# Kernel optimization log

Measured on AMD Instinct MI355X. Metric: run time of the kernel, lower is better.

## Reference

```python
import jax, jax.numpy as jnp
import numpy as np
import math

V, B, C, H, W, D, G, N = 4, 2, 32, 128, 128, 32, 8, 4
ATTN_TEMP = 2.0


def _bilinear_sample(img, gx, gy):
    """img: (C,Hs,Ws); gx,gy: (P,) normalized coords in [-1,1].
    PyTorch grid_sample(mode=bilinear, padding=zeros, align_corners=True)."""
    Cc, Hs, Ws = img.shape
    x = (gx + 1.0) * 0.5 * (Ws - 1)
    y = (gy + 1.0) * 0.5 * (Hs - 1)
    x0 = jnp.floor(x)
    y0 = jnp.floor(y)
    wx = x - x0
    wy = y - y0
    x0i = x0.astype(jnp.int32)
    y0i = y0.astype(jnp.int32)

    def gather(xi, yi):
        valid = ((xi >= 0) & (xi < Ws) & (yi >= 0) & (yi < Hs)).astype(img.dtype)
        v = img[:, jnp.clip(yi, 0, Hs - 1), jnp.clip(xi, 0, Ws - 1)]
        return v * valid

    v00 = gather(x0i, y0i)
    v01 = gather(x0i + 1, y0i)
    v10 = gather(x0i, y0i + 1)
    v11 = gather(x0i + 1, y0i + 1)
    return (v00 * (1 - wx) + v01 * wx) * (1 - wy) + (v10 * (1 - wx) + v11 * wx) * wy


_bilinear_batched = jax.vmap(_bilinear_sample)  # over batch


def _homo_warp(src_fea, src_proj, ref_proj, depth):
    """src_fea (B,C,Hs,Ws), projs (B,4,4), depth (B,D,H,W) -> (B,C,D,H,W)."""
    Bb, Cc, Hs, Ws = src_fea.shape
    Dd, Hr, Wr = depth.shape[1], depth.shape[2], depth.shape[3]
    proj = src_proj @ jnp.linalg.inv(ref_proj)
    rot = proj[:, :3, :3]
    trans = proj[:, :3, 3]  # (B,3)
    yy, xx = jnp.meshgrid(jnp.arange(Hr, dtype=jnp.float32),
                          jnp.arange(Wr, dtype=jnp.float32), indexing='ij')
    xyz = jnp.stack([xx.ravel(), yy.ravel(), jnp.ones(Hr * Wr, jnp.float32)], 0)  # (3,P)
    rot_xyz = jnp.einsum('bij,jp->bip', rot, xyz)  # (B,3,P)
    pts = rot_xyz[:, :, None, :] * depth.reshape(Bb, 1, Dd, Hr * Wr) \
          + trans[:, :, None, None]  # (B,3,D,P)
    z = pts[:, 2]
    z = jnp.where(z == 0.0, 1e-9, z)
    gx = pts[:, 0] / z / ((Ws - 1) / 2.0) - 1.0  # (B,D,P)
    gy = pts[:, 1] / z / ((Hs - 1) / 2.0) - 1.0
    # grid built under torch.no_grad in the original
    gx = jax.lax.stop_gradient(gx).reshape(Bb, Dd * Hr * Wr)
    gy = jax.lax.stop_gradient(gy).reshape(Bb, Dd * Hr * Wr)
    warped = _bilinear_batched(src_fea, gx, gy)  # (B,C,D*P)
    return warped.reshape(Bb, Cc, Dd, Hr, Wr)


def setup_inputs() -> dict:
    key = jax.random.key(0)
    ks = jax.random.split(key, 6)
    ref_features = jax.random.normal(ks[0], (V, B, C, H, W), jnp.float32)
    src_features = jax.random.normal(ks[1], (V, B, C, H, W), jnp.float32)
    # structured camera matrices: [.,.,0]=extrinsic, [.,.,1]=intrinsic
    f = 100.0
    K = np.eye(4, dtype=np.float32)
    K[0, 0] = f; K[1, 1] = f; K[0, 2] = W / 2.0; K[1, 2] = H / 2.0
    projs = np.zeros((B, V + 1, 2, 4, 4), np.float32)
    for v in range(V + 1):
        ang = 0.0 if v == 0 else 0.02 * v
        ca, sa = math.cos(ang), math.sin(ang)
        E = np.eye(4, dtype=np.float32)
        E[:3, :3] = np.array([[ca, 0, sa], [0, 1, 0], [-sa, 0, ca]], np.float32)
        E[0, 3] = 0.0 if v == 0 else 5.0 * v
        projs[:, v, 0] = E
        projs[:, v, 1] = K
    proj_matrices = jnp.asarray(projs)
    dvals = jnp.linspace(425.0, 935.0, D, dtype=jnp.float32)
    depth_hypo = dvals[None, :, None, None] * jnp.ones((B, D, H, W), jnp.float32)
    sample_grids = 2.0 * jax.random.uniform(ks[2], (V, B, N, H, W, 2), jnp.float32) - 1.0
    w_reg = jax.random.normal(ks[3], (G,), jnp.float32) * 0.1
    w_enh = jax.random.normal(ks[4], (G, G * N), jnp.float32) * 0.05
    return {
        'ref_features': ref_features,
        'src_features': src_features,
        'proj_matrices': proj_matrices,
        'depth_hypo': depth_hypo,
        'sample_grids': sample_grids,
        'w_reg': w_reg,
        'w_enh': w_enh,
        'group_cor_dim': G,
        'stage_idx': 3,
    }


def reference(ref_features, src_features, proj_matrices, depth_hypo,
              sample_grids, w_reg, w_enh, group_cor_dim, stage_idx):
    Bb, Dd, Hh, Ww = depth_hypo.shape
    Cc = ref_features.shape[2]
    Gg = group_cor_dim
    ref_proj = proj_matrices[:, 0]
    ref_proj_new = ref_proj[:, 0].at[:, :3, :4].set(
        jnp.einsum('bij,bjk->bik', ref_proj[:, 1, :3, :3], ref_proj[:, 0, :3, :4]))
    cor_weight_sum = 1e-8
    cor_feats = 0.0
    cor_weights = []
    for src_idx in range(V):
        src_proj = proj_matrices[:, src_idx + 1]
        src_proj_new = src_proj[:, 0].at[:, :3, :4].set(
            jnp.einsum('bij,bjk->bik', src_proj[:, 1, :3, :3], src_proj[:, 0, :3, :4]))
        warped_src = _homo_warp(src_features[src_idx], src_proj_new, ref_proj_new,
                                depth_hypo)  # (B,C,D,H,W)
        ref_vol = ref_features[src_idx][:, :, None].reshape(Bb, Gg, Cc // Gg, 1, Hh, Ww)
        wsrc = warped_src.reshape(Bb, Gg, Cc // Gg, Dd, Hh, Ww)
        cor_feat = (wsrc * ref_vol).mean(2)  # (B,G,D,H,W) group correlation
        # --- regcorr: second grid_sample along epipolar-line samples ---
        cf = cor_feat.reshape(Bb, Gg * Dd, Hh, Ww)
        grids = sample_grids[src_idx].reshape(Bb, N * Hh * Ww, 2)
        cf_s = _bilinear_batched(cf, grids[..., 0], grids[..., 1])  # (B,G*D,N*H*W)
        cf_s = cf_s.reshape(Bb, Gg, Dd, N, Hh, Ww)
        cf_s = jnp.transpose(cf_s, (0, 1, 3, 2, 4, 5)).reshape(Bb, Gg * N, Dd, Hh, Ww)
        # line_cross_enhanced_net stand-in: learned mix of line samples, residual add
        cor_feat = cor_feat + jnp.einsum('gk,bkdhw->bgdhw', w_enh, cf_s)
        # --- attn_fuse_d softmax fusion across depth ---
        cor_weight = jax.nn.softmax(cor_feat.sum(1) / ATTN_TEMP, axis=1) / math.sqrt(Cc)
        cor_weight_sum = cor_weight_sum + cor_weight
        cor_weights.append(cor_weight.max(1))
        cor_feats = cor_feats + cor_weight[:, None] * cor_feat
    cor_feats = cor_feats / cor_weight_sum[:, None]
    # regnet stand-in: linear reduction over group dim
    attn_logits = jnp.einsum('g,bgdhw->bdhw', w_reg, cor_feats)
    attn_weight = jax.nn.softmax(attn_logits, axis=1)
    idx = jnp.argmax(attn_weight, axis=1)  # (B,H,W)
    depth = jnp.take_along_axis(depth_hypo, idx[:, None], axis=1)[:, 0]
    # stage_idx=3 -> interpolate scale_factor=1 (identity)
    photometric_confidence = attn_weight.max(1)
    return depth, photometric_confidence, attn_weight, jnp.stack(cor_weights)
```

## Files before the change

kernel.cpp:

```cpp
#include <hip/hip_runtime.h>

#define Vv 4
#define Bn 2
#define Cn 32
#define Hn 128
#define Wn 128
#define Dn 32
#define Gn 8
#define Nn 4
#define HW (Hn*Wn)
#define BHW (Bn*Hn*Wn)
#define DHW (Dn*Hn*Wn)
#define BDHW (Bn*Dn*Hn*Wn)
#define NBLK (DHW/256)
#define WBLK (DHW/512)
#define RBLK (Gn*HW/256)
#define NST  (Vv*Bn)

__global__ void setup_proj(const float* __restrict__ pm,
                           const float* __restrict__ wenh,
                           const float* __restrict__ wreg,
                           double* __restrict__ projws,
                           double* __restrict__ wtab) {
    int t = threadIdx.x;
    if (t < Gn) wtab[t] = (double)wreg[t];
    if (t < Gn * Nn) {
        double a = 0.0, c = 0.0;
        for (int g = 0; g < Gn; g++) {
            double wv = (double)wenh[g * (Gn * Nn) + t];
            a += wv;
            c += (double)wreg[g] * wv;
        }
        wtab[8 + t] = a; wtab[40 + t] = c;
    }
    if (t >= Vv * Bn) return;
    int v = t / Bn, b = t % Bn;
    const float* Eref = pm + (((size_t)b * (Vv + 1) + 0) * 2 + 0) * 16;
    const float* Kref = pm + (((size_t)b * (Vv + 1) + 0) * 2 + 1) * 16;
    const float* Esrc = pm + (((size_t)b * (Vv + 1) + (v + 1)) * 2 + 0) * 16;
    const float* Ksrc = pm + (((size_t)b * (Vv + 1) + (v + 1)) * 2 + 1) * 16;
    double R[16], S[16];
    for (int r = 0; r < 3; r++)
        for (int c = 0; c < 4; c++) {
            R[r*4+c] = (double)Kref[r*4+0]*Eref[0*4+c] + (double)Kref[r*4+1]*Eref[1*4+c] + (double)Kref[r*4+2]*Eref[2*4+c];
            S[r*4+c] = (double)Ksrc[r*4+0]*Esrc[0*4+c] + (double)Ksrc[r*4+1]*Esrc[1*4+c] + (double)Ksrc[r*4+2]*Esrc[2*4+c];
        }
    for (int c = 0; c < 4; c++) { R[12+c] = Eref[12+c]; S[12+c] = Esrc[12+c]; }
    double M[4][8];
    for (int r = 0; r < 4; r++)
        for (int c = 0; c < 4; c++) { M[r][c] = R[r*4+c]; M[r][4+c] = (r == c) ? 1.0 : 0.0; }
    for (int col = 0; col < 4; col++) {
        int piv = col; double best = fabs(M[col][col]);
        for (int r = col+1; r < 4; r++) { double a = fabs(M[r][col]); if (a > best) { best = a; piv = r; } }
        if (piv != col)
            for (int c = 0; c < 8; c++) { double tmp = M[col][c]; M[col][c] = M[piv][c]; M[piv][c] = tmp; }
        double inv = 1.0 / M[col][col];
        for (int c = 0; c < 8; c++) M[col][c] *= inv;
        for (int r = 0; r < 4; r++) if (r != col) {
            double f = M[r][col];
            for (int c = 0; c < 8; c++) M[r][c] -= f * M[col][c];
        }
    }
    double P[16];
    for (int r = 0; r < 4; r++)
        for (int c = 0; c < 4; c++) {
            double acc = 0.0;
            for (int k = 0; k < 4; k++) acc += S[r*4+k] * M[k][4+c];
            P[r*4+c] = acc;
        }
    double* o = projws + t * 12;
    o[0]=P[0];  o[1]=P[1];  o[2]=P[2];
    o[3]=P[4];  o[4]=P[5];  o[5]=P[6];
    o[6]=P[8];  o[7]=P[9];  o[8]=P[10];
    o[9]=P[3];  o[10]=P[7]; o[11]=P[11];
}

__device__ __forceinline__ void repack_body(
    int tid, const float* __restrict__ srcf, const float* __restrict__ reff,
    float4* __restrict__ qsrc, float4* __restrict__ qref, int v, int b)
{
    int p = tid & (HW - 1);
    int g = tid >> 14;
    const float* sb = srcf + ((size_t)(v*Bn + b)) * Cn * HW + (size_t)(g*4) * HW + p;
    const float* rb = reff + ((size_t)(v*Bn + b)) * Cn * HW + (size_t)(g*4) * HW + p;
    float4 s4; s4.x = sb[0]; s4.y = sb[HW]; s4.z = sb[2*HW]; s4.w = sb[3*HW];
    float4 r4; r4.x = rb[0]; r4.y = rb[HW]; r4.z = rb[2*HW]; r4.w = rb[3*HW];
    qsrc[(size_t)g * HW + p] = s4;
    qref[(size_t)g * HW + p] = r4;
}

__device__ __forceinline__ void warp_bin_q(
    int d, int p, double bx, double by, double bz,
    const float4* __restrict__ qsrc, const float4* __restrict__ qref,
    const float* __restrict__ dh, const double* __restrict__ pr,
    const float* sU1, const float* sU2, const float* sR,
    float2* __restrict__ ownbuf, float2* __restrict__ tapbuf, int b)
{
    double depth = (double)dh[(size_t)(b * Dn + d) * HW + p];
    double px = bx * depth + pr[9];
    double py = by * depth + pr[10];
    double pz = bz * depth + pr[11];
    if (pz == 0.0) pz = 1e-9;
    double invz = 1.0 / pz;
    double xs = px * invz;
    double ys = py * invz;
    double x0f = floor(xs), y0f = floor(ys);
    double wx = xs - x0f, wy = ys - y0f;
    int ix = (int)x0f, iy = (int)y0f;
    bool vx0 = (ix >= 0) && (ix < Wn), vx1 = (ix + 1 >= 0) && (ix + 1 < Wn);
    bool vy0 = (iy >= 0) && (iy < Hn), vy1 = (iy + 1 >= 0) && (iy + 1 < Hn);
    int cx0 = min(max(ix, 0), Wn-1), cx1 = min(max(ix+1, 0), Wn-1);
    int cy0 = min(max(iy, 0), Hn-1), cy1 = min(max(iy+1, 0), Hn-1);
    float a00 = (vx0 && vy0) ? (float)((1.0-wx)*(1.0-wy)) : 0.f;
    float a01 = (vx1 && vy0) ? (float)(wx*(1.0-wy))       : 0.f;
    float a10 = (vx0 && vy1) ? (float)((1.0-wx)*wy)       : 0.f;
    float a11 = (vx1 && vy1) ? (float)(wx*wy)             : 0.f;
    int o00 = cy0*Wn + cx0, o01 = cy0*Wn + cx1, o10 = cy1*Wn + cx0, o11 = cy1*Wn + cx1;
    float cor[Gn];
    #pragma unroll
    for (int half = 0; half < 2; half++) {
        float4 T00[4], T01[4], T10[4], T11[4];
        #pragma unroll
        for (int j2 = 0; j2 < 4; j2++) {
            const float4* qs = qsrc + (size_t)(half*4 + j2) * HW;
            T00[j2] = qs[o00]; T01[j2] = qs[o01];
            T10[j2] = qs[o10]; T11[j2] = qs[o11];
        }
        #pragma unroll
        for (int j2 = 0; j2 < 4; j2++) {
            int j = half*4 + j2;
            float4 rr = qref[(size_t)j * HW + p];
            float vx = a00*T00[j2].x + a01*T01[j2].x + a10*T10[j2].x + a11*T11[j2].x;
            float vy = a00*T00[j2].y + a01*T01[j2].y + a10*T10[j2].y + a11*T11[j2].y;
            float vz = a00*T00[j2].z + a01*T01[j2].z + a10*T10[j2].z + a11*T11[j2].z;
            float vw = a00*T00[j2].w + a01*T01[j2].w + a10*T10[j2].w + a11*T11[j2].w;
            cor[j] = ((vx*rr.x + vy*rr.y) + vz*rr.z) + vw*rr.w;
        }
    }
    float s_own = 0.f, r_own = 0.f;
    #pragma unroll
    for (int g = 0; g < Gn; g++) { s_own += cor[g]; r_own += sR[g] * cor[g]; }
    float2 o2; o2.x = 0.25f * s_own; o2.y = 0.25f * r_own;
    ownbuf[(size_t)p * Dn + d] = o2;
    #pragma unroll
    for (int n = 0; n < Nn; n++) {
        float t1 = 0.f, t2 = 0.f;
        #pragma unroll
        for (int g = 0; g < Gn; g++) {
            t1 += sU1[g*Nn + n] * cor[g];
            t2 += sU2[g*Nn + n] * cor[g];
        }
        float2 t; t.x = 0.25f * t1; t.y = 0.25f * t2;
        tapbuf[((size_t)p * Nn + n) * Dn + d] = t;
    }
}

__device__ __forceinline__ void warp_body_q2(
    int tid, const float4* __restrict__ qsrc, const float4* __restrict__ qref,
    const float* __restrict__ dh, const double* __restrict__ projws,
    const float* sU1, const float* sU2, const float* sR,
    float2* __restrict__ ownbuf, float2* __restrict__ tapbuf, int v, int b)
{
    int dlo = tid & 15, p = tid >> 4;
    int w = p & 127, h = p >> 7;
    const double* pr = projws + (v * Bn + b) * 12;
    double xf = (double)w, yf = (double)h;
    double bx = pr[0]*xf + pr[1]*yf + pr[2];
    double by = pr[3]*xf + pr[4]*yf + pr[5];
    double bz = pr[6]*xf + pr[7]*yf + pr[8];
    #pragma unroll
    for (int e = 0; e < 2; e++)
        warp_bin_q(dlo + 16*e, p, bx, by, bz, qsrc, qref, dh, pr,
                   sU1, sU2, sR, ownbuf, tapbuf, b);
}

__device__ __forceinline__ void warp_body(
    int tid, const float* __restrict__ srcf, const float* __restrict__ reff,
    const float* __restrict__ dh, const double* __restrict__ projws,
    const float* sU1, const float* sU2, const float* sR,
    float2* __restrict__ ownbuf, float2* __restrict__ tapbuf, int v, int b)
{
    int d = tid & 31, p = tid >> 5;
    int w = p & 127, h = p >> 7;
    const double* pr = projws + (v * Bn + b) * 12;
    double depth = (double)dh[(size_t)(b * Dn + d) * HW + p];
    double xf = (double)w, yf = (double)h;
    double px = (pr[0]*xf + pr[1]*yf + pr[2]) * depth + pr[9];
    double py = (pr[3]*xf + pr[4]*yf + pr[5]) * depth + pr[10];
    double pz = (pr[6]*xf + pr[7]*yf + pr[8]) * depth + pr[11];
    if (pz == 0.0) pz = 1e-9;
    double invz = 1.0 / pz;
    double xs = px * invz;
    double ys = py * invz;
    double x0f = floor(xs), y0f = floor(ys);
    double wx = xs - x0f, wy = ys - y0f;
    int ix = (int)x0f, iy = (int)y0f;
    bool vx0 = (ix >= 0) && (ix < Wn), vx1 = (ix + 1 >= 0) && (ix + 1 < Wn);
    bool vy0 = (iy >= 0) && (iy < Hn), vy1 = (iy + 1 >= 0) && (iy + 1 < Hn);
    int cx0 = min(max(ix, 0), Wn-1), cx1 = min(max(ix+1, 0), Wn-1);
    int cy0 = min(max(iy, 0), Hn-1), cy1 = min(max(iy+1, 0), Hn-1);
    float a00 = (vx0 && vy0) ? (float)((1.0-wx)*(1.0-wy)) : 0.f;
    float a01 = (vx1 && vy0) ? (float)(wx*(1.0-wy))       : 0.f;
    float a10 = (vx0 && vy1) ? (float)((1.0-wx)*wy)       : 0.f;
    float a11 = (vx1 && vy1) ? (float)(wx*wy)             : 0.f;
    int o00 = cy0*Wn + cx0, o01 = cy0*Wn + cx1, o10 = cy1*Wn + cx0, o11 = cy1*Wn + cx1;
    const float* sb = srcf + ((size_t)(v*Bn + b)) * Cn * HW;
    const float* rb = reff + ((size_t)(v*Bn + b)) * Cn * HW + p;
    float cor[Gn];
    #pragma unroll
    for (int g = 0; g < Gn; g++) cor[g] = 0.f;
    #pragma unroll
    for (int c = 0; c < Cn; c++) {
        const float* sc = sb + c * HW;
        float val = a00*sc[o00] + a01*sc[o01] + a10*sc[o10] + a11*sc[o11];
        cor[c >> 2] += val * rb[c * HW];
    }
    float s_own = 0.f, r_own = 0.f;
    #pragma unroll
    for (int g = 0; g < Gn; g++) { s_own += cor[g]; r_own += sR[g] * cor[g]; }
    float2 o2; o2.x = 0.25f * s_own; o2.y = 0.25f * r_own;
    ownbuf[tid] = o2;
    #pragma unroll
    for (int n = 0; n < Nn; n++) {
        float t1 = 0.f, t2 = 0.f;
        #pragma unroll
        for (int g = 0; g < Gn; g++) {
            t1 += sU1[g*Nn + n] * cor[g];
            t2 += sU2[g*Nn + n] * cor[g];
        }
        float2 t; t.x = 0.25f * t1; t.y = 0.25f * t2;
        tapbuf[((size_t)p * Nn + n) * Dn + d] = t;
    }
}

__device__ __forceinline__ void sample_view(
    int d, int p, int w, int h,
    const float2* __restrict__ ownbuf, const float2* __restrict__ tapbuf,
    const float* __restrict__ grids, float* __restrict__ out_corw,
    int v, int b, double& cw_out, double& r_out)
{
    float2 ow = ownbuf[(size_t)p * Dn + d];
    double s = (double)ow.x, r = (double)ow.y;
    const float2* gb2 = (const float2*)(grids + ((size_t)(v*Bn + b)) * Nn * HW * 2);
    #pragma unroll
    for (int n = 0; n < Nn; n++) {
        float2 g2 = gb2[((size_t)n * Hn + h) * Wn + w];
        double gx = (double)g2.x, gy = (double)g2.y;
        double xs = (gx + 1.0) * 63.5;
        double ys = (gy + 1.0) * 63.5;
        double x0f = floor(xs), y0f = floor(ys);
        double wx = xs - x0f, wy = ys - y0f;
        int ix = (int)x0f, iy = (int)y0f;
        bool vx0 = (ix >= 0) && (ix < Wn), vx1 = (ix + 1 >= 0) && (ix + 1 < Wn);
        bool vy0 = (iy >= 0) && (iy < Hn), vy1 = (iy + 1 >= 0) && (iy + 1 < Hn);
        int cx0 = min(max(ix, 0), Wn-1), cx1 = min(max(ix+1, 0), Wn-1);
        int cy0 = min(max(iy, 0), Hn-1), cy1 = min(max(iy+1, 0), Hn-1);
        double a00 = (vx0 && vy0) ? (1.0-wx)*(1.0-wy) : 0.0;
        double a01 = (vx1 && vy0) ? wx*(1.0-wy)       : 0.0;
        double a10 = (vx0 && vy1) ? (1.0-wx)*wy       : 0.0;
        double a11 = (vx1 && vy1) ? wx*wy             : 0.0;
        float2 q00 = tapbuf[((size_t)(cy0*Wn + cx0) * Nn + n) * Dn + d];
        float2 q01 = tapbuf[((size_t)(cy0*Wn + cx1) * Nn + n) * Dn + d];
        float2 q10 = tapbuf[((size_t)(cy1*Wn + cx0) * Nn + n) * Dn + d];
        float2 q11 = tapbuf[((size_t)(cy1*Wn + cx1) * Nn + n) * Dn + d];
        s += a00*(double)q00.x + a01*(double)q01.x + a10*(double)q10.x + a11*(double)q11.x;
        r += a00*(double)q00.y + a01*(double)q01.y + a10*(double)q10.y + a11*(double)q11.y;
    }
    double logit = s * 0.5;
    double m = logit;
    #pragma unroll
    for (int mask = 16; mask >= 1; mask >>= 1) m = fmax(m, __shfl_xor(m, mask));
    double e = exp(logit - m);
    double ssum = e;
    #pragma unroll
    for (int mask = 16; mask >= 1; mask >>= 1) ssum += __shfl_xor(ssum, mask);
    const double SQRTC = 5.656854249492381;
    if (d == 0) out_corw[(size_t)v * BHW + (size_t)b * HW + p] = (float)(1.0 / ssum / SQRTC);
    cw_out = e / ssum / SQRTC;
    r_out = r;
}

__device__ __forceinline__ void finalize_core(
    int d, int p, int b, double cs, double wr,
    const float* __restrict__ depth_hypo, float* __restrict__ out)
{
    double lg = wr / cs;
    double fm = lg;
    #pragma unroll
    for (int mask = 16; mask >= 1; mask >>= 1) fm = fmax(fm, __shfl_xor(fm, mask));
    double fe = exp(lg - fm);
    double fsum = fe;
    #pragma unroll
    for (int mask = 16; mask >= 1; mask >>= 1) fsum += __shfl_xor(fsum, mask);
    out[2*BHW + (size_t)b * DHW + (size_t)d * HW + p] = (float)(fe / fsum);
    double bv = lg; int bi = d;
    #pragma unroll
    for (int mask = 16; mask >= 1; mask >>= 1) {
        double ov = __shfl_xor(bv, mask);
        int oi = __shfl_xor(bi, mask);
        if (ov > bv || (ov == bv && oi < bi)) { bv = ov; bi = oi; }
    }
    double rv = (d == bi) ? -1e300 : lg; int ri = d;
    #pragma unroll
    for (int mask = 16; mask >= 1; mask >>= 1) {
        double ov = __shfl_xor(rv, mask);
        int oi = __shfl_xor(ri, mask);
        if (ov > rv || (ov == rv && oi < ri)) { rv = ov; ri = oi; }
    }
    if (d == 0) {
        const float* dhb = depth_hypo + (size_t)b * DHW + p;
        double eps = 5e-3 * (1.0 + fabs(bv));
        bool adj = (ri == bi + 1) || (ri == bi - 1);
        float dep;
        if (adj && (bv - rv) <= eps)
            dep = 0.5f * (dhb[(size_t)bi * HW] + dhb[(size_t)ri * HW]);
        else
            dep = dhb[(size_t)bi * HW];
        out[(size_t)b * HW + p] = dep;
        out[BHW + (size_t)b * HW + p] = (float)(1.0 / fsum);
    }
}

__global__ __launch_bounds__(256) void mega_repack(
    const float* __restrict__ srcf, const float* __restrict__ reff,
    float4* __restrict__ qs_all, float4* __restrict__ qr_all)
{
    int s = blockIdx.x >> 9;
    int tid = (blockIdx.x & 511) * 256 + threadIdx.x;
    int v = s & 3, b = s >> 2;
    repack_body(tid, srcf, reff, qs_all + (size_t)s * Gn * HW,
                qr_all + (size_t)s * Gn * HW, v, b);
}

__global__ __launch_bounds__(256) void mega_warp(
    const float4* __restrict__ qs_all, const float4* __restrict__ qr_all,
    const float* __restrict__ dh, const double* __restrict__ projws,
    const double* __restrict__ wtab,
    float2* __restrict__ own_all, float2* __restrict__ tap_all)
{
    __shared__ float sU1[Gn * Nn], sU2[Gn * Nn], sR[Gn];
    int lt = threadIdx.x;
    if (lt < Gn * Nn) { sU1[lt] = (float)wtab[8 + lt]; sU2[lt] = (float)wtab[40 + lt]; }
    if (lt < Gn) sR[lt] = (float)wtab[lt];
    __syncthreads();
    int s = blockIdx.x >> 10;
    int tid = (blockIdx.x & 1023) * 256 + lt;
    int v = s & 3, b = s >> 2;
    warp_body_q2(tid, qs_all + (size_t)s * Gn * HW, qr_all + (size_t)s * Gn * HW,
                 dh, projws, sU1, sU2, sR,
                 own_all + (size_t)s * DHW, tap_all + (size_t)s * Nn * DHW, v, b);
}

__global__ __launch_bounds__(256) void mega_sample(
    const float2* __restrict__ own_all, const float2* __restrict__ tap_all,
    const float* __restrict__ grids, const float* __restrict__ dh,
    float* __restrict__ out_corw, float* __restrict__ out)
{
    int tid = blockIdx.x * 256 + threadIdx.x;
    int d = tid & 31;
    int p = (tid >> 5) & (HW - 1);
    int b = tid >> 19;
    int w = p & 127, h = p >> 7;
    double cs = 1e-8, wr = 0.0;
    for (int v = 0; v < Vv; v++) {
        int s = b * 4 + v;
        double cw, r;
        sample_view(d, p, w, h, own_all + (size_t)s * DHW,
                    tap_all + (size_t)s * Nn * DHW, grids, out_corw, v, b, cw, r);
        cs += cw;
        wr += cw * r;
    }
    finalize_core(d, p, b, cs, wr, dh, out);
}

template <int MODE>
__device__ __forceinline__ void sample_body(
    int tid, const float2* __restrict__ ownbuf, const float2* __restrict__ tapbuf,
    const float* __restrict__ grids, float2* __restrict__ accf,
    float* __restrict__ out_corw, const float* __restrict__ depth_hypo,
    float* __restrict__ out, int v, int b)
{
    int d = tid & 31;
    int p = tid >> 5;
    int w = p & 127, h = p >> 7;
    double cw, r;
    sample_view(d, p, w, h, ownbuf, tapbuf, grids, out_corw, v, b, cw, r);
    if (MODE == 0) {
        float2 a; a.x = (float)(1e-8 + cw); a.y = (float)(cw * r);
        accf[tid] = a;
    } else if (MODE == 1) {
        float2 a = accf[tid];
        a.x = (float)((double)a.x + cw);
        a.y = (float)((double)a.y + cw * r);
        accf[tid] = a;
    } else {
        float2 a = accf[tid];
        finalize_core(d, p, b, (double)a.x + cw, (double)a.y + cw * r, depth_hypo, out);
    }
}

__global__ __launch_bounds__(256) void warp_corr(
    const float* __restrict__ srcf, const float* __restrict__ reff,
    const float* __restrict__ dh, const double* __restrict__ projws,
    const double* __restrict__ wtab,
    float2* __restrict__ ownbuf, float2* __restrict__ tapbuf, int v, int b)
{
    __shared__ float sU1[Gn * Nn], sU2[Gn * Nn], sR[Gn];
    int lt = threadIdx.x;
    if (lt < Gn * Nn) { sU1[lt] = (float)wtab[8 + lt]; sU2[lt] = (float)wtab[40 + lt]; }
    if (lt < Gn) sR[lt] = (float)wtab[lt];
    __syncthreads();
    warp_body(blockIdx.x * 256 + lt, srcf, reff, dh, projws, sU1, sU2, sR,
              ownbuf, tapbuf, v, b);
}

template <int MODE>
__global__ __launch_bounds__(256) void sample_enh(
    const float2* __restrict__ ownbuf, const float2* __restrict__ tapbuf,
    const float* __restrict__ grids, float2* __restrict__ accf,
    float* __restrict__ out_corw, const float* __restrict__ depth_hypo,
    float* __restrict__ out, int v, int b)
{
    sample_body<MODE>(blockIdx.x * 256 + threadIdx.x, ownbuf, tapbuf, grids,
                      accf, out_corw, depth_hypo, out, v, b);
}

template <int MODE>
__global__ __launch_bounds__(256) void fused_sw(
    const float* __restrict__ srcf, const float* __restrict__ reff,
    const float* __restrict__ dh, const double* __restrict__ projws,
    const double* __restrict__ wtab, const float* __restrict__ grids,
    const float2* __restrict__ ownR, const float2* __restrict__ tapR,
    float2* __restrict__ ownW, float2* __restrict__ tapW,
    float2* __restrict__ accf, float* __restrict__ out_corw,
    float* __restrict__ out, int vs, int bs, int vw, int bw)
{
    int lt = threadIdx.x;
    int role = blockIdx.x & 1;
    int vb   = blockIdx.x >> 1;
    if (role == 0) {
        sample_body<MODE>(vb * 256 + lt, ownR, tapR, grids,
                          accf, out_corw, dh, out, vs, bs);
    } else {
        __shared__ float sU1[Gn * Nn], sU2[Gn * Nn], sR[Gn];
        if (lt < Gn * Nn) { sU1[lt] = (float)wtab[8 + lt]; sU2[lt] = (float)wtab[40 + lt]; }
        if (lt < Gn) sR[lt] = (float)wtab[lt];
        __syncthreads();
        warp_body(vb * 256 + lt, srcf, reff, dh, projws,
                  sU1, sU2, sR, ownW, tapW, vw, bw);
    }
}

extern "C" void kernel_launch(void* const* d_in, const int* in_sizes, int n_in,
                              void* d_out, int out_size, void* d_ws, size_t ws_size,
                              hipStream_t stream) {
    const float* reff  = (const float*)d_in[0];
    const float* srcf  = (const float*)d_in[1];
    const float* pm    = (const float*)d_in[2];
    const float* dh    = (const float*)d_in[3];
    const float* grids = (const float*)d_in[4];
    const float* wreg  = (const float*)d_in[5];
    const float* wenh  = (const float*)d_in[6];
    float* out = (float*)d_out;
    double* projws = (double*)d_ws;
    double* wtab   = (double*)((char*)d_ws + 1024);
    char*   base   = (char*)d_ws + 2048;
    float2* tap_all = (float2*)base;
    float2* own_all = tap_all + (size_t)NST * Nn * DHW;
    float4* qs_all  = (float4*)(own_all + (size_t)NST * DHW);
    float4* qr_all  = qs_all + (size_t)NST * Gn * HW;
    size_t need_mega = 2048 + (size_t)NST * Nn * DHW * 8 + (size_t)NST * DHW * 8
                     + 2 * (size_t)NST * Gn * HW * 16;
    float2* accf = (float2*)base;
    float2* own0 = accf + DHW;
    float2* tap0 = own0 + DHW;
    float2* own1 = tap0 + (size_t)DHW * Nn;
    float2* tap1 = own1 + DHW;
    size_t need_pipe = 2048 + (size_t)DHW * 8 + 2 * ((size_t)DHW * 8 + (size_t)DHW * Nn * 8);

    setup_proj<<<1, 64, 0, stream>>>(pm, wenh, wreg, projws, wtab);
    float* out_corw = out + 2*BHW + BDHW;

    if (ws_size >= need_mega) {
        mega_repack<<<NST * RBLK, 256, 0, stream>>>(srcf, reff, qs_all, qr_all);
        mega_warp<<<NST * WBLK, 256, 0, stream>>>(qs_all, qr_all, dh, projws, wtab,
                                                  own_all, tap_all);
        mega_sample<<<BDHW / 256, 256, 0, stream>>>(own_all, tap_all, grids, dh,
                                                    out_corw, out);
    } else if (ws_size >= need_pipe) {
        float2* owns[2] = { own0, own1 };
        float2* taps[2] = { tap0, tap1 };
        warp_corr<<<NBLK, 256, 0, stream>>>(srcf, reff, dh, projws, wtab,
                                            own0, tap0, 0, 0);
        for (int k = 1; k < 8; k++) {
            int vs = (k - 1) & 3, bs = (k - 1) >> 2;
            int vw = k & 3,       bw = k >> 2;
            float2* oR = owns[(k - 1) & 1]; float2* tR = taps[(k - 1) & 1];
            float2* oW = owns[k & 1];       float2* tW = taps[k & 1];
            if (vs == 0)
                fused_sw<0><<<2*NBLK, 256, 0, stream>>>(srcf, reff, dh, projws, wtab, grids,
                                                        oR, tR, oW, tW, accf,
                                                        out_corw, out, vs, bs, vw, bw);
            else if (vs == 3)
                fused_sw<2><<<2*NBLK, 256, 0, stream>>>(srcf, reff, dh, projws, wtab, grids,
                                                        oR, tR, oW, tW, accf,
                                                        out_corw, out, vs, bs, vw, bw);
            else
                fused_sw<1><<<2*NBLK, 256, 0, stream>>>(srcf, reff, dh, projws, wtab, grids,
                                                        oR, tR, oW, tW, accf,
                                                        out_corw, out, vs, bs, vw, bw);
        }
        sample_enh<2><<<NBLK, 256, 0, stream>>>(owns[1], taps[1], grids, accf,
                                                out_corw, dh, out, 3, 1);
    } else {
        for (int b = 0; b < Bn; b++) {
            for (int v = 0; v < Vv; v++) {
                warp_corr<<<NBLK, 256, 0, stream>>>(srcf, reff, dh, projws, wtab,
                                                    own0, tap0, v, b);
                if (v == 0)
                    sample_enh<0><<<NBLK, 256, 0, stream>>>(own0, tap0, grids, accf,
                                                            out_corw, dh, out, v, b);
                else if (v < Vv - 1)
                    sample_enh<1><<<NBLK, 256, 0, stream>>>(own0, tap0, grids, accf,
                                                            out_corw, dh, out, v, b);
                else
                    sample_enh<2><<<NBLK, 256, 0, stream>>>(own0, tap0, grids, accf,
                                                            out_corw, dh, out, v, b);
            }
        }
    }
}
```

Measured before the change: 185.0 us.

## Split warp/sample into half-stage phases and overlap sampling with warping

Warping is split into two launches covering views {0,1} and {2,3}. A fused kernel interleaves blocks that sample views 0-1 (accumulating partial sums into a new workspace buffer) with blocks that warp views 2-3, so gather-bound and compute-bound work run concurrently. A final kernel finishes sampling views 2-3 from the stored partials. The warp body also loads the reference features once per pixel for both depth bins rather than per bin, at the cost of more registers and an extra launch plus accumulator traffic.

```diff
diff --git a/kernel.cpp b/kernel.cpp
--- a/kernel.cpp
+++ b/kernel.cpp
@@ -15,6 +15,7 @@
 #define NBLK (DHW/256)
 #define WBLK (DHW/512)
 #define RBLK (Gn*HW/256)
+#define SBLK (BDHW/256)
 #define NST  (Vv*Bn)
 
 __global__ void setup_proj(const float* __restrict__ pm,
@@ -89,12 +90,11 @@
     qref[(size_t)g * HW + p] = r4;
 }
 
-__device__ __forceinline__ void warp_bin_q(
+__device__ __forceinline__ void warp_gather(
     int d, int p, double bx, double by, double bz,
-    const float4* __restrict__ qsrc, const float4* __restrict__ qref,
+    const float4* __restrict__ qsrc, const float4 rr[Gn],
     const float* __restrict__ dh, const double* __restrict__ pr,
-    const float* sU1, const float* sU2, const float* sR,
-    float2* __restrict__ ownbuf, float2* __restrict__ tapbuf, int b)
+    int b, float cor[Gn])
 {
     double depth = (double)dh[(size_t)(b * Dn + d) * HW + p];
     double px = bx * depth + pr[9];
@@ -116,7 +116,6 @@
     float a10 = (vx0 && vy1) ? (float)((1.0-wx)*wy)       : 0.f;
     float a11 = (vx1 && vy1) ? (float)(wx*wy)             : 0.f;
     int o00 = cy0*Wn + cx0, o01 = cy0*Wn + cx1, o10 = cy1*Wn + cx0, o11 = cy1*Wn + cx1;
-    float cor[Gn];
     #pragma unroll
     for (int half = 0; half < 2; half++) {
         float4 T00[4], T01[4], T10[4], T11[4];
@@ -129,29 +128,12 @@
         #pragma unroll
         for (int j2 = 0; j2 < 4; j2++) {
             int j = half*4 + j2;
-            float4 rr = qref[(size_t)j * HW + p];
             float vx = a00*T00[j2].x + a01*T01[j2].x + a10*T10[j2].x + a11*T11[j2].x;
             float vy = a00*T00[j2].y + a01*T01[j2].y + a10*T10[j2].y + a11*T11[j2].y;
             float vz = a00*T00[j2].z + a01*T01[j2].z + a10*T10[j2].z + a11*T11[j2].z;
             float vw = a00*T00[j2].w + a01*T01[j2].w + a10*T10[j2].w + a11*T11[j2].w;
-            cor[j] = ((vx*rr.x + vy*rr.y) + vz*rr.z) + vw*rr.w;
-        }
-    }
-    float s_own = 0.f, r_own = 0.f;
-    #pragma unroll
-    for (int g = 0; g < Gn; g++) { s_own += cor[g]; r_own += sR[g] * cor[g]; }
-    float2 o2; o2.x = 0.25f * s_own; o2.y = 0.25f * r_own;
-    ownbuf[(size_t)p * Dn + d] = o2;
-    #pragma unroll
-    for (int n = 0; n < Nn; n++) {
-        float t1 = 0.f, t2 = 0.f;
-        #pragma unroll
-        for (int g = 0; g < Gn; g++) {
-            t1 += sU1[g*Nn + n] * cor[g];
-            t2 += sU2[g*Nn + n] * cor[g];
-        }
-        float2 t; t.x = 0.25f * t1; t.y = 0.25f * t2;
-        tapbuf[((size_t)p * Nn + n) * Dn + d] = t;
+            cor[j] = ((vx*rr[j].x + vy*rr[j].y) + vz*rr[j].z) + vw*rr[j].w;
+        }
     }
 }
 
@@ -168,10 +150,36 @@
     double bx = pr[0]*xf + pr[1]*yf + pr[2];
     double by = pr[3]*xf + pr[4]*yf + pr[5];
     double bz = pr[6]*xf + pr[7]*yf + pr[8];
-    #pragma unroll
-    for (int e = 0; e < 2; e++)
-        warp_bin_q(dlo + 16*e, p, bx, by, bz, qsrc, qref, dh, pr,
-                   sU1, sU2, sR, ownbuf, tapbuf, b);
+    float4 rr[Gn];
+    #pragma unroll
+    for (int j = 0; j < Gn; j++) rr[j] = qref[(size_t)j * HW + p];
+    float cor0[Gn], cor1[Gn];
+    warp_gather(dlo,      p, bx, by, bz, qsrc, rr, dh, pr, b, cor0);
+    warp_gather(dlo + 16, p, bx, by, bz, qsrc, rr, dh, pr, b, cor1);
+    float s0 = 0.f, r0 = 0.f, s1 = 0.f, r1 = 0.f;
+    #pragma unroll
+    for (int g = 0; g < Gn; g++) {
+        s0 += cor0[g]; r0 += sR[g] * cor0[g];
+        s1 += cor1[g]; r1 += sR[g] * cor1[g];
+    }
+    float2 o0; o0.x = 0.25f * s0; o0.y = 0.25f * r0;
+    float2 o1; o1.x = 0.25f * s1; o1.y = 0.25f * r1;
+    ownbuf[(size_t)p * Dn + dlo]      = o0;
+    ownbuf[(size_t)p * Dn + dlo + 16] = o1;
+    #pragma unroll
+    for (int n = 0; n < Nn; n++) {
+        float t10 = 0.f, t20 = 0.f, t11_ = 0.f, t21 = 0.f;
+        #pragma unroll
+        for (int g = 0; g < Gn; g++) {
+            float u1 = sU1[g*Nn + n], u2 = sU2[g*Nn + n];
+            t10 += u1 * cor0[g]; t20 += u2 * cor0[g];
+            t11_ += u1 * cor1[g]; t21 += u2 * cor1[g];
+        }
+        float2 t0; t0.x = 0.25f * t10; t0.y = 0.25f * t20;
+        float2 t1; t1.x = 0.25f * t11_; t1.y = 0.25f * t21;
+        tapbuf[((size_t)p * Nn + n) * Dn + dlo]      = t0;
+        tapbuf[((size_t)p * Nn + n) * Dn + dlo + 16] = t1;
+    }
 }
 
 __device__ __forceinline__ void warp_body(
@@ -332,18 +340,19 @@
                 qr_all + (size_t)s * Gn * HW, v, b);
 }
 
-__global__ __launch_bounds__(256) void mega_warp(
+__global__ __launch_bounds__(256) void mega_warp4(
     const float4* __restrict__ qs_all, const float4* __restrict__ qr_all,
     const float* __restrict__ dh, const double* __restrict__ projws,
     const double* __restrict__ wtab,
-    float2* __restrict__ own_all, float2* __restrict__ tap_all)
+    float2* __restrict__ own_all, float2* __restrict__ tap_all, int4 stages)
 {
     __shared__ float sU1[Gn * Nn], sU2[Gn * Nn], sR[Gn];
     int lt = threadIdx.x;
     if (lt < Gn * Nn) { sU1[lt] = (float)wtab[8 + lt]; sU2[lt] = (float)wtab[40 + lt]; }
     if (lt < Gn) sR[lt] = (float)wtab[lt];
     __syncthreads();
-    int s = blockIdx.x >> 10;
+    int si = blockIdx.x >> 10;
+    int s = (si == 0) ? stages.x : (si == 1) ? stages.y : (si == 2) ? stages.z : stages.w;
     int tid = (blockIdx.x & 1023) * 256 + lt;
     int v = s & 3, b = s >> 2;
     warp_body_q2(tid, qs_all + (size_t)s * Gn * HW, qr_all + (size_t)s * Gn * HW,
@@ -351,18 +360,71 @@
                  own_all + (size_t)s * DHW, tap_all + (size_t)s * Nn * DHW, v, b);
 }
 
-__global__ __launch_bounds__(256) void mega_sample(
+__device__ __forceinline__ void sample1_body(
+    int tid, const float2* __restrict__ own_all, const float2* __restrict__ tap_all,
+    const float* __restrict__ grids, float2* __restrict__ accf,
+    float* __restrict__ out_corw)
+{
+    int d = tid & 31;
+    int p = (tid >> 5) & (HW - 1);
+    int b = tid >> 19;
+    int w = p & 127, h = p >> 7;
+    double cs = 1e-8, wr = 0.0;
+    #pragma unroll
+    for (int v = 0; v < 2; v++) {
+        int s = b * 4 + v;
+        double cw, r;
+        sample_view(d, p, w, h, own_all + (size_t)s * DHW,
+                    tap_all + (size_t)s * Nn * DHW, grids, out_corw, v, b, cw, r);
+        cs += cw;
+        wr += cw * r;
+    }
+    float2 a; a.x = (float)cs; a.y = (float)wr;
+    accf[tid] = a;
+}
+
+__global__ __launch_bounds__(256) void fused_s1wB(
+    const float4* __restrict__ qs_all, const float4* __restrict__ qr_all,
+    const float* __restrict__ dh, const double* __restrict__ projws,
+    const double* __restrict__ wtab, const float* __restrict__ grids,
+    float2* __restrict__ own_all, float2* __restrict__ tap_all,
+    float2* __restrict__ accf, float* __restrict__ out_corw, int4 stagesB)
+{
+    int lt = threadIdx.x;
+    int role = blockIdx.x & 1;
+    int vb   = blockIdx.x >> 1;
+    if (role == 0) {
+        sample1_body(vb * 256 + lt, own_all, tap_all, grids, accf, out_corw);
+    } else {
+        __shared__ float sU1[Gn * Nn], sU2[Gn * Nn], sR[Gn];
+        if (lt < Gn * Nn) { sU1[lt] = (float)wtab[8 + lt]; sU2[lt] = (float)wtab[40 + lt]; }
+        if (lt < Gn) sR[lt] = (float)wtab[lt];
+        __syncthreads();
+        int si = vb >> 10;
+        int s = (si == 0) ? stagesB.x : (si == 1) ? stagesB.y : (si == 2) ? stagesB.z : stagesB.w;
+        int tid = (vb & 1023) * 256 + lt;
+        int v = s & 3, b = s >> 2;
+        warp_body_q2(tid, qs_all + (size_t)s * Gn * HW, qr_all + (size_t)s * Gn * HW,
+                     dh, projws, sU1, sU2, sR,
+                     own_all + (size_t)s * DHW, tap_all + (size_t)s * Nn * DHW, v, b);
+    }
+}
+
+__global__ __launch_bounds__(256) void mega_sample2(
     const float2* __restrict__ own_all, const float2* __restrict__ tap_all,
     const float* __restrict__ grids, const float* __restrict__ dh,
-    float* __restrict__ out_corw, float* __restrict__ out)
+    const float2* __restrict__ accf, float* __restrict__ out_corw,
+    float* __restrict__ out)
 {
     int tid = blockIdx.x * 256 + threadIdx.x;
     int d = tid & 31;
     int p = (tid >> 5) & (HW - 1);
     int b = tid >> 19;
     int w = p & 127, h = p >> 7;
-    double cs = 1e-8, wr = 0.0;
-    for (int v = 0; v < Vv; v++) {
+    float2 a = accf[tid];
+    double cs = (double)a.x, wr = (double)a.y;
+    #pragma unroll
+    for (int v = 2; v < 4; v++) {
         int s = b * 4 + v;
         double cw, r;
         sample_view(d, p, w, h, own_all + (size_t)s * DHW,
@@ -469,8 +531,9 @@
     float2* own_all = tap_all + (size_t)NST * Nn * DHW;
     float4* qs_all  = (float4*)(own_all + (size_t)NST * DHW);
     float4* qr_all  = qs_all + (size_t)NST * Gn * HW;
+    float2* accm    = (float2*)(qr_all + (size_t)NST * Gn * HW);
     size_t need_mega = 2048 + (size_t)NST * Nn * DHW * 8 + (size_t)NST * DHW * 8
-                     + 2 * (size_t)NST * Gn * HW * 16;
+                     + 2 * (size_t)NST * Gn * HW * 16 + (size_t)BDHW * 8;
     float2* accf = (float2*)base;
     float2* own0 = accf + DHW;
     float2* tap0 = own0 + DHW;
@@ -482,11 +545,16 @@
     float* out_corw = out + 2*BHW + BDHW;
 
     if (ws_size >= need_mega) {
+        int4 stagesA = make_int4(0, 1, 4, 5);
+        int4 stagesB = make_int4(2, 3, 6, 7);
         mega_repack<<<NST * RBLK, 256, 0, stream>>>(srcf, reff, qs_all, qr_all);
-        mega_warp<<<NST * WBLK, 256, 0, stream>>>(qs_all, qr_all, dh, projws, wtab,
-                                                  own_all, tap_all);
-        mega_sample<<<BDHW / 256, 256, 0, stream>>>(own_all, tap_all, grids, dh,
-                                                    out_corw, out);
+        mega_warp4<<<4 * WBLK, 256, 0, stream>>>(qs_all, qr_all, dh, projws, wtab,
+                                                 own_all, tap_all, stagesA);
+        fused_s1wB<<<2 * SBLK, 256, 0, stream>>>(qs_all, qr_all, dh, projws, wtab,
+                                                 grids, own_all, tap_all, accm,
+                                                 out_corw, stagesB);
+        mega_sample2<<<SBLK, 256, 0, stream>>>(own_all, tap_all, grids, dh, accm,
+                                               out_corw, out);
     } else if (ws_size >= need_pipe) {
         float2* owns[2] = { own0, own1 };
         float2* taps[2] = { tap0, tap1 };
```

Result: slower. 224.9 us (+21.6%).
